# Performance work log

Hardware: AMD Instinct MI355X
Metric: run time of the kernel (lower is better)

Reference implementation:

```python
import jax, jax.numpy as jnp
import numpy as np
import math

N = 8192
F_DIM = 128
ALPHA_SLOPE = 0.2  # LeakyReLU negative slope from __init__ alpha


def setup_inputs() -> dict:
    key = jax.random.key(0)
    k1, k2, k3, k4, k5 = jax.random.split(key, 5)
    inp = jax.random.normal(k1, (N, F_DIM), dtype=jnp.float32)
    adj = (jax.random.uniform(k2, (N, N)) < 0.02).astype(jnp.float32)
    adj = adj.at[jnp.arange(N), jnp.arange(N)].set(1.0)
    h0 = jax.random.normal(k3, (N, F_DIM), dtype=jnp.float32)
    W = jax.random.normal(k4, (F_DIM, F_DIM), dtype=jnp.float32) * (1.414 * math.sqrt(6.0 / (2 * F_DIM)))
    a = jax.random.normal(k5, (2 * F_DIM, 1), dtype=jnp.float32) * (1.414 * math.sqrt(6.0 / (2 * F_DIM + 1)))
    return {"inp": inp, "adj": adj, "h0": h0, "W": W, "a": a,
            "lamda": 0.5, "alpha_mix": 0.1, "l": 1}


def reference(inp, adj, h0, W, a, lamda, alpha_mix, l):
    # h = inp @ W  -> (N, F)
    h = inp @ W
    # score(i,j) = leakyrelu([h_i, h_j] @ a) = leakyrelu(h_i@a1 + h_j@a2)
    # avoids materializing the O(N^2 * 2F) a_input tensor of the original
    f1 = h @ a[:F_DIM, 0]   # (N,)
    f2 = h @ a[F_DIM:, 0]   # (N,)
    e = jax.nn.leaky_relu(f1[:, None] + f2[None, :], negative_slope=ALPHA_SLOPE)  # (N, N)
    e = jnp.where(adj > 0, e, jnp.float32(-1e12))
    attention = jax.nn.softmax(e, axis=1)
    # dropout skipped (inference / training=False)
    hi = attention @ inp                      # (N, F) -- note: aggregates inp, not h
    support = (1.0 - alpha_mix) * hi + alpha_mix * h0
    theta = min(1.0, math.log(lamda / l + 1.0))
    output = theta * (support @ W) + (1.0 - theta) * support + inp
    return output
```

## Files before the change

### kernel.cpp

```cpp
#include <hip/hip_runtime.h>
#include <math.h>

#define N 8192
#define F 128
#define SLOPE 0.2f
#define SEGCAP 96
#define RPB 4

typedef float f4v __attribute__((ext_vector_type(4)));

__device__ __forceinline__ float lrelu(float x) { return x > 0.0f ? x : SLOPE * x; }

__device__ __forceinline__ f4v ntload(const float* p) {
    return __builtin_nontemporal_load(reinterpret_cast<const f4v*>(p));
}

__device__ __forceinline__ int mbcnt64(unsigned long long m) {
    return __builtin_amdgcn_mbcnt_hi((unsigned)(m >> 32),
                                     __builtin_amdgcn_mbcnt_lo((unsigned)m, 0u));
}

__device__ __forceinline__ unsigned bf16pair(float a, float b) {
    unsigned ua = __builtin_bit_cast(unsigned, a);
    unsigned ub = __builtin_bit_cast(unsigned, b);
    ua = (ua + 0x7FFFu + ((ua >> 16) & 1u)) >> 16;
    ub = (ub + 0x7FFFu + ((ub >> 16) & 1u)) >> 16;
    return ua | (ub << 16);
}
__device__ __forceinline__ float bflo(unsigned u) {
    return __builtin_bit_cast(float, u << 16);
}
__device__ __forceinline__ float bfhi(unsigned u) {
    return __builtin_bit_cast(float, u & 0xFFFF0000u);
}

__global__ __launch_bounds__(128) void k_wa(const float* __restrict__ W,
                                            const float* __restrict__ a,
                                            float* __restrict__ Wa1,
                                            float* __restrict__ Wa2) {
    const int k = threadIdx.x;
    const float* wr = W + k * F;
    float s1 = 0.f, s2 = 0.f;
    #pragma unroll 8
    for (int j = 0; j < F; ++j) {
        float w = wr[j];
        s1 += w * a[j];
        s2 += w * a[F + j];
    }
    Wa1[k] = s1;
    Wa2[k] = s2;
}

__global__ __launch_bounds__(256) void k_f(const float* __restrict__ inp,
                                           const float* __restrict__ Wa1,
                                           const float* __restrict__ Wa2,
                                           float* __restrict__ f1,
                                           float* __restrict__ f2,
                                           unsigned* __restrict__ inpb) {
    const int lane = threadIdx.x & 63;
    const int wv = threadIdx.x >> 6;
    const int i = blockIdx.x * 4 + wv;
    const float2 xv = *reinterpret_cast<const float2*>(inp + (size_t)i * F + 2 * lane);
    const float2 w1v = *reinterpret_cast<const float2*>(Wa1 + 2 * lane);
    const float2 w2v = *reinterpret_cast<const float2*>(Wa2 + 2 * lane);
    float v1 = xv.x * w1v.x + xv.y * w1v.y;
    float v2 = xv.x * w2v.x + xv.y * w2v.y;
    #pragma unroll
    for (int off = 32; off; off >>= 1) {
        v1 += __shfl_xor(v1, off);
        v2 += __shfl_xor(v2, off);
    }
    if (lane == 0) { f1[i] = v1; f2[i] = v2; }
    inpb[i * 64 + lane] = bf16pair(xv.x, xv.y);
}

__global__ __launch_bounds__(1024) void k_max(const float* __restrict__ f2,
                                              float* __restrict__ f2max) {
    float m = -INFINITY;
    for (int idx = threadIdx.x; idx < N; idx += 1024) m = fmaxf(m, f2[idx]);
    #pragma unroll
    for (int off = 32; off; off >>= 1) m = fmaxf(m, __shfl_xor(m, off));
    __shared__ float s[16];
    if ((threadIdx.x & 63) == 0) s[threadIdx.x >> 6] = m;
    __syncthreads();
    if (threadIdx.x == 0) {
        float r = s[0];
        #pragma unroll
        for (int t = 1; t < 16; ++t) r = fmaxf(r, s[t]);
        *f2max = r;
    }
}

__global__ __launch_bounds__(256, 8) void k_compact(const float* __restrict__ adj,
                                                    int* __restrict__ nzidx,
                                                    int* __restrict__ nzcnt) {
    const int row = blockIdx.x;
    const int wv = threadIdx.x >> 6;
    const int lane = threadIdx.x & 63;

    __shared__ int s_seg[4][SEGCAP];

    const float* base = adj + (size_t)row * N + wv * 2048 + lane * 4;
    f4v v[8];
    #pragma unroll
    for (int u = 0; u < 8; ++u) v[u] = ntload(base + u * 256);

    int cnt = 0;
    #pragma unroll
    for (int u = 0; u < 8; ++u) {
        const int col0 = wv * 2048 + u * 256 + lane * 4;
        #pragma unroll
        for (int c = 0; c < 4; ++c) {
            const bool nz = v[u][c] > 0.f;
            const unsigned long long m = __ballot(nz);
            const int pos = mbcnt64(m);
            int p = cnt + pos;
            if (p > SEGCAP - 1) p = SEGCAP - 1;
            if (nz) s_seg[wv][p] = col0 + c;
            cnt += (int)__popcll(m);
        }
    }
    const int M = cnt > SEGCAP ? SEGCAP : cnt;
    int* seg = nzidx + ((size_t)row * 4 + wv) * SEGCAP;
    for (int t2 = lane; t2 < M; t2 += 64) seg[t2] = s_seg[wv][t2];
    if (lane == 0) nzcnt[row * 4 + wv] = M;
}

__global__ __launch_bounds__(256, 8) void k_agg(const int* __restrict__ nzidx,
                                                const int* __restrict__ nzcnt,
                                                const unsigned* __restrict__ inpb,
                                                const float* __restrict__ inp,
                                                const float* __restrict__ h0,
                                                const float* __restrict__ W,
                                                const float* __restrict__ f1,
                                                const float* __restrict__ f2,
                                                const float* __restrict__ f2max_p,
                                                const float* __restrict__ lamda_p,
                                                const float* __restrict__ alpha_p,
                                                const int* __restrict__ l_p,
                                                float* __restrict__ out) {
    const int r0 = blockIdx.x * RPB;
    const int t = threadIdx.x;
    const int lane = t & 63;
    const int wv = t >> 6;
    const int i = r0 + wv;

    __shared__ int   s_j[RPB][392];
    __shared__ float s_w[RPB][392];
    __shared__ float s_sup[RPB][F];
    __shared__ float s_dot[RPB][F];

    const float f1i = f1[i];
    const float bound = lrelu(f1i + *f2max_p);

    int total = 0;
    float wlane = 0.f;
    #pragma unroll
    for (int s = 0; s < 4; ++s) {
        const int cnt = nzcnt[i * 4 + s];
        const int* seg = nzidx + ((size_t)i * 4 + s) * SEGCAP;
        const int e2 = 64 + lane;
        const int j1 = (lane < cnt) ? seg[lane] : -1;
        const int j2 = (e2 < cnt) ? seg[e2] : -1;
        float w1 = 0.f, w2 = 0.f;
        if (j1 >= 0) w1 = __expf(lrelu(f1i + f2[j1]) - bound);
        if (j2 >= 0) w2 = __expf(lrelu(f1i + f2[j2]) - bound);
        if (j1 >= 0) { s_j[wv][total + lane] = j1; s_w[wv][total + lane] = w1; }
        if (j2 >= 0) { s_j[wv][total + e2] = j2; s_w[wv][total + e2] = w2; }
        wlane += w1 + w2;
        total += cnt;
    }
    if (lane < 4) { s_j[wv][total + lane] = 0; s_w[wv][total + lane] = 0.f; }
    float wsum = wlane;
    #pragma unroll
    for (int off = 32; off; off >>= 1) wsum += __shfl_xor(wsum, off);

    float acc_e = 0.f, acc_o = 0.f;
    for (int e = 0; e < total; e += 4) {
        const int4  jv = *reinterpret_cast<const int4*>(&s_j[wv][e]);
        const f4v   wq = *reinterpret_cast<const f4v*>(&s_w[wv][e]);
        const unsigned a0 = inpb[(size_t)jv.x * 64 + lane];
        const unsigned a1 = inpb[(size_t)jv.y * 64 + lane];
        const unsigned a2 = inpb[(size_t)jv.z * 64 + lane];
        const unsigned a3 = inpb[(size_t)jv.w * 64 + lane];
        acc_e = fmaf(wq[0], bflo(a0), acc_e); acc_o = fmaf(wq[0], bfhi(a0), acc_o);
        acc_e = fmaf(wq[1], bflo(a1), acc_e); acc_o = fmaf(wq[1], bfhi(a1), acc_o);
        acc_e = fmaf(wq[2], bflo(a2), acc_e); acc_o = fmaf(wq[2], bfhi(a2), acc_o);
        acc_e = fmaf(wq[3], bflo(a3), acc_e); acc_o = fmaf(wq[3], bfhi(a3), acc_o);
    }

    const float inv = 1.0f / wsum;
    const float alpha = *alpha_p;
    const float2 hv = *reinterpret_cast<const float2*>(h0 + (size_t)i * F + 2 * lane);
    const float sup_e = (1.0f - alpha) * (acc_e * inv) + alpha * hv.x;
    const float sup_o = (1.0f - alpha) * (acc_o * inv) + alpha * hv.y;
    s_sup[wv][2 * lane]     = sup_e;
    s_sup[wv][2 * lane + 1] = sup_o;
    __syncthreads();

    const int c = t & 127;
    const int h = t >> 7;
    float d0 = 0.f, d1 = 0.f, d2 = 0.f, d3 = 0.f;
    const int k0 = 64 * h;
    #pragma unroll 4
    for (int k = k0; k < k0 + 64; ++k) {
        const float wk = W[k * F + c];
        d0 = fmaf(s_sup[0][k], wk, d0);
        d1 = fmaf(s_sup[1][k], wk, d1);
        d2 = fmaf(s_sup[2][k], wk, d2);
        d3 = fmaf(s_sup[3][k], wk, d3);
    }
    if (h == 0) {
        s_dot[0][c] = d0; s_dot[1][c] = d1; s_dot[2][c] = d2; s_dot[3][c] = d3;
    }
    __syncthreads();
    if (h == 1) {
        const float lam = *lamda_p;
        const float th = fminf(1.0f, logf(lam / (float)(*l_p) + 1.0f));
        const float dr[4] = { d0 + s_dot[0][c], d1 + s_dot[1][c],
                              d2 + s_dot[2][c], d3 + s_dot[3][c] };
        #pragma unroll
        for (int r = 0; r < RPB; ++r) {
            const size_t o = (size_t)(r0 + r) * F + c;
            out[o] = th * dr[r] + (1.0f - th) * s_sup[r][c] + inp[o];
        }
    }
}

extern "C" void kernel_launch(void* const* d_in, const int* in_sizes, int n_in,
                              void* d_out, int out_size, void* d_ws, size_t ws_size,
                              hipStream_t stream) {
    const float* inp   = (const float*)d_in[0];
    const float* adj   = (const float*)d_in[1];
    const float* h0    = (const float*)d_in[2];
    const float* W     = (const float*)d_in[3];
    const float* a     = (const float*)d_in[4];
    const float* lamda = (const float*)d_in[5];
    const float* alpha = (const float*)d_in[6];
    const int*   l     = (const int*)d_in[7];
    float* out = (float*)d_out;

    float* ws  = (float*)d_ws;
    float*    Wa1   = ws;
    float*    Wa2   = ws + F;
    float*    f1    = ws + 2 * F;
    float*    f2    = ws + 2 * F + N;
    float*    f2m   = ws + 2 * F + 2 * N;
    int*      nzcnt = (int*)(ws + 16704);
    int*      nzidx = (int*)(ws + 49472);
    unsigned* inpb  = (unsigned*)(ws + 3195200);

    hipLaunchKernelGGL(k_wa, dim3(1), dim3(F), 0, stream, W, a, Wa1, Wa2);
    hipLaunchKernelGGL(k_f, dim3(N / 4), dim3(256), 0, stream, inp, Wa1, Wa2, f1, f2, inpb);
    hipLaunchKernelGGL(k_max, dim3(1), dim3(1024), 0, stream, f2, f2m);
    hipLaunchKernelGGL(k_compact, dim3(N), dim3(256), 0, stream, adj, nzidx, nzcnt);
    hipLaunchKernelGGL(k_agg, dim3(N / RPB), dim3(256), 0, stream,
                       nzidx, nzcnt, inpb, inp, h0, W, f1, f2, f2m, lamda, alpha, l, out);
}
```

Baseline: 97.48 us.

## Merge compaction and feature-projection kernels, compute per-row softmax max in aggregation

The adjacency compaction and the f1/f2/bf16 projection kernels are fused into one launch, with block index selecting the role. The global f2 max reduction kernel is removed, and each row now computes its exact softmax max from its own neighbour scores before exponentiating. The k_wa kernel is parallelised over 256 threads using vector loads. The gather loop is unrolled to 8 neighbours per iteration, and the occupancy hint for k_agg is lowered. These changes cut launch count and serial single-block kernels at the cost of an extra max pass and more registers in the aggregation kernel.

```diff
diff --git a/kernel.cpp b/kernel.cpp
--- a/kernel.cpp
+++ b/kernel.cpp
@@ -34,99 +34,79 @@
     return __builtin_bit_cast(float, u & 0xFFFF0000u);
 }
 
-__global__ __launch_bounds__(128) void k_wa(const float* __restrict__ W,
+__global__ __launch_bounds__(256) void k_wa(const float* __restrict__ W,
                                             const float* __restrict__ a,
-                                            float* __restrict__ Wa1,
-                                            float* __restrict__ Wa2) {
-    const int k = threadIdx.x;
-    const float* wr = W + k * F;
-    float s1 = 0.f, s2 = 0.f;
-    #pragma unroll 8
-    for (int j = 0; j < F; ++j) {
-        float w = wr[j];
-        s1 += w * a[j];
-        s2 += w * a[F + j];
-    }
-    Wa1[k] = s1;
-    Wa2[k] = s2;
-}
-
-__global__ __launch_bounds__(256) void k_f(const float* __restrict__ inp,
-                                           const float* __restrict__ Wa1,
-                                           const float* __restrict__ Wa2,
-                                           float* __restrict__ f1,
-                                           float* __restrict__ f2,
-                                           unsigned* __restrict__ inpb) {
-    const int lane = threadIdx.x & 63;
-    const int wv = threadIdx.x >> 6;
-    const int i = blockIdx.x * 4 + wv;
-    const float2 xv = *reinterpret_cast<const float2*>(inp + (size_t)i * F + 2 * lane);
-    const float2 w1v = *reinterpret_cast<const float2*>(Wa1 + 2 * lane);
-    const float2 w2v = *reinterpret_cast<const float2*>(Wa2 + 2 * lane);
-    float v1 = xv.x * w1v.x + xv.y * w1v.y;
-    float v2 = xv.x * w2v.x + xv.y * w2v.y;
-    #pragma unroll
-    for (int off = 32; off; off >>= 1) {
-        v1 += __shfl_xor(v1, off);
-        v2 += __shfl_xor(v2, off);
-    }
-    if (lane == 0) { f1[i] = v1; f2[i] = v2; }
-    inpb[i * 64 + lane] = bf16pair(xv.x, xv.y);
-}
-
-__global__ __launch_bounds__(1024) void k_max(const float* __restrict__ f2,
-                                              float* __restrict__ f2max) {
-    float m = -INFINITY;
-    for (int idx = threadIdx.x; idx < N; idx += 1024) m = fmaxf(m, f2[idx]);
-    #pragma unroll
-    for (int off = 32; off; off >>= 1) m = fmaxf(m, __shfl_xor(m, off));
-    __shared__ float s[16];
-    if ((threadIdx.x & 63) == 0) s[threadIdx.x >> 6] = m;
-    __syncthreads();
-    if (threadIdx.x == 0) {
-        float r = s[0];
-        #pragma unroll
-        for (int t = 1; t < 16; ++t) r = fmaxf(r, s[t]);
-        *f2max = r;
-    }
-}
-
-__global__ __launch_bounds__(256, 8) void k_compact(const float* __restrict__ adj,
-                                                    int* __restrict__ nzidx,
-                                                    int* __restrict__ nzcnt) {
-    const int row = blockIdx.x;
+                                            float* __restrict__ Wa) {
+    const int t = threadIdx.x;
+    const int k = t & 127;
+    const int half = t >> 7;
+    const f4v* wr = reinterpret_cast<const f4v*>(W + k * F);
+    const f4v* av = reinterpret_cast<const f4v*>(a + half * F);
+    float s = 0.f;
+    #pragma unroll
+    for (int q = 0; q < 32; ++q) {
+        const f4v w = wr[q], aa = av[q];
+        s += (w[0] * aa[0] + w[1] * aa[1]) + (w[2] * aa[2] + w[3] * aa[3]);
+    }
+    Wa[t] = s;
+}
+
+__global__ __launch_bounds__(256, 8) void k_main(const float* __restrict__ adj,
+                                                 const float* __restrict__ inp,
+                                                 const float* __restrict__ Wa,
+                                                 float* __restrict__ f1,
+                                                 float* __restrict__ f2,
+                                                 unsigned* __restrict__ inpb,
+                                                 int* __restrict__ nzidx,
+                                                 int* __restrict__ nzcnt) {
+    __shared__ int s_seg[4][SEGCAP];
+    const int bid = blockIdx.x;
     const int wv = threadIdx.x >> 6;
     const int lane = threadIdx.x & 63;
 
-    __shared__ int s_seg[4][SEGCAP];
-
-    const float* base = adj + (size_t)row * N + wv * 2048 + lane * 4;
-    f4v v[8];
-    #pragma unroll
-    for (int u = 0; u < 8; ++u) v[u] = ntload(base + u * 256);
-
-    int cnt = 0;
-    #pragma unroll
-    for (int u = 0; u < 8; ++u) {
-        const int col0 = wv * 2048 + u * 256 + lane * 4;
-        #pragma unroll
-        for (int c = 0; c < 4; ++c) {
-            const bool nz = v[u][c] > 0.f;
-            const unsigned long long m = __ballot(nz);
-            const int pos = mbcnt64(m);
-            int p = cnt + pos;
-            if (p > SEGCAP - 1) p = SEGCAP - 1;
-            if (nz) s_seg[wv][p] = col0 + c;
-            cnt += (int)__popcll(m);
-        }
-    }
-    const int M = cnt > SEGCAP ? SEGCAP : cnt;
-    int* seg = nzidx + ((size_t)row * 4 + wv) * SEGCAP;
-    for (int t2 = lane; t2 < M; t2 += 64) seg[t2] = s_seg[wv][t2];
-    if (lane == 0) nzcnt[row * 4 + wv] = M;
-}
-
-__global__ __launch_bounds__(256, 8) void k_agg(const int* __restrict__ nzidx,
+    if (bid < N) {
+        const float* base = adj + (size_t)bid * N + wv * 2048 + lane * 4;
+        f4v v[8];
+        #pragma unroll
+        for (int u = 0; u < 8; ++u) v[u] = ntload(base + u * 256);
+
+        int cnt = 0;
+        #pragma unroll
+        for (int u = 0; u < 8; ++u) {
+            const int col0 = wv * 2048 + u * 256 + lane * 4;
+            #pragma unroll
+            for (int c = 0; c < 4; ++c) {
+                const bool nz = v[u][c] > 0.f;
+                const unsigned long long m = __ballot(nz);
+                const int pos = mbcnt64(m);
+                int p = cnt + pos;
+                if (p > SEGCAP - 1) p = SEGCAP - 1;
+                if (nz) s_seg[wv][p] = col0 + c;
+                cnt += (int)__popcll(m);
+            }
+        }
+        const int M = cnt > SEGCAP ? SEGCAP : cnt;
+        int* seg = nzidx + ((size_t)bid * 4 + wv) * SEGCAP;
+        for (int t2 = lane; t2 < M; t2 += 64) seg[t2] = s_seg[wv][t2];
+        if (lane == 0) nzcnt[bid * 4 + wv] = M;
+    } else {
+        const int i = (bid - N) * 4 + wv;
+        const float2 xv = *reinterpret_cast<const float2*>(inp + (size_t)i * F + 2 * lane);
+        const float2 w1v = *reinterpret_cast<const float2*>(Wa + 2 * lane);
+        const float2 w2v = *reinterpret_cast<const float2*>(Wa + F + 2 * lane);
+        float v1 = xv.x * w1v.x + xv.y * w1v.y;
+        float v2 = xv.x * w2v.x + xv.y * w2v.y;
+        #pragma unroll
+        for (int off = 32; off; off >>= 1) {
+            v1 += __shfl_xor(v1, off);
+            v2 += __shfl_xor(v2, off);
+        }
+        if (lane == 0) { f1[i] = v1; f2[i] = v2; }
+        inpb[i * 64 + lane] = bf16pair(xv.x, xv.y);
+    }
+}
+
+__global__ __launch_bounds__(256, 4) void k_agg(const int* __restrict__ nzidx,
                                                 const int* __restrict__ nzcnt,
                                                 const unsigned* __restrict__ inpb,
                                                 const float* __restrict__ inp,
@@ -134,7 +114,6 @@
                                                 const float* __restrict__ W,
                                                 const float* __restrict__ f1,
                                                 const float* __restrict__ f2,
-                                                const float* __restrict__ f2max_p,
                                                 const float* __restrict__ lamda_p,
                                                 const float* __restrict__ alpha_p,
                                                 const int* __restrict__ l_p,
@@ -145,48 +124,74 @@
     const int wv = t >> 6;
     const int i = r0 + wv;
 
-    __shared__ int   s_j[RPB][392];
-    __shared__ float s_w[RPB][392];
+    __shared__ int   s_j[RPB][400];
+    __shared__ float s_w[RPB][400];
     __shared__ float s_sup[RPB][F];
     __shared__ float s_dot[RPB][F];
 
     const float f1i = f1[i];
-    const float bound = lrelu(f1i + *f2max_p);
+
+    int cnts[4], jA[4], jB[4];
+    float sA[4], sB[4];
+    float mx = -1e30f;
+    #pragma unroll
+    for (int s = 0; s < 4; ++s) {
+        cnts[s] = nzcnt[i * 4 + s];
+        const int* seg = nzidx + ((size_t)i * 4 + s) * SEGCAP;
+        jA[s] = (lane < cnts[s]) ? seg[lane] : -1;
+        jB[s] = (64 + lane < cnts[s]) ? seg[64 + lane] : -1;
+        sA[s] = (jA[s] >= 0) ? lrelu(f1i + f2[jA[s]]) : -1e30f;
+        sB[s] = (jB[s] >= 0) ? lrelu(f1i + f2[jB[s]]) : -1e30f;
+        mx = fmaxf(mx, fmaxf(sA[s], sB[s]));
+    }
+    #pragma unroll
+    for (int off = 32; off; off >>= 1) mx = fmaxf(mx, __shfl_xor(mx, off));
 
     int total = 0;
     float wlane = 0.f;
     #pragma unroll
     for (int s = 0; s < 4; ++s) {
-        const int cnt = nzcnt[i * 4 + s];
-        const int* seg = nzidx + ((size_t)i * 4 + s) * SEGCAP;
-        const int e2 = 64 + lane;
-        const int j1 = (lane < cnt) ? seg[lane] : -1;
-        const int j2 = (e2 < cnt) ? seg[e2] : -1;
         float w1 = 0.f, w2 = 0.f;
-        if (j1 >= 0) w1 = __expf(lrelu(f1i + f2[j1]) - bound);
-        if (j2 >= 0) w2 = __expf(lrelu(f1i + f2[j2]) - bound);
-        if (j1 >= 0) { s_j[wv][total + lane] = j1; s_w[wv][total + lane] = w1; }
-        if (j2 >= 0) { s_j[wv][total + e2] = j2; s_w[wv][total + e2] = w2; }
+        if (jA[s] >= 0) {
+            w1 = __expf(sA[s] - mx);
+            s_j[wv][total + lane] = jA[s];
+            s_w[wv][total + lane] = w1;
+        }
+        if (jB[s] >= 0) {
+            w2 = __expf(sB[s] - mx);
+            s_j[wv][total + 64 + lane] = jB[s];
+            s_w[wv][total + 64 + lane] = w2;
+        }
         wlane += w1 + w2;
-        total += cnt;
-    }
-    if (lane < 4) { s_j[wv][total + lane] = 0; s_w[wv][total + lane] = 0.f; }
+        total += cnts[s];
+    }
+    if (lane < 8) { s_j[wv][total + lane] = 0; s_w[wv][total + lane] = 0.f; }
     float wsum = wlane;
     #pragma unroll
     for (int off = 32; off; off >>= 1) wsum += __shfl_xor(wsum, off);
 
     float acc_e = 0.f, acc_o = 0.f;
-    for (int e = 0; e < total; e += 4) {
-        const int4  jv = *reinterpret_cast<const int4*>(&s_j[wv][e]);
-        const f4v   wq = *reinterpret_cast<const f4v*>(&s_w[wv][e]);
-        const unsigned a0 = inpb[(size_t)jv.x * 64 + lane];
-        const unsigned a1 = inpb[(size_t)jv.y * 64 + lane];
-        const unsigned a2 = inpb[(size_t)jv.z * 64 + lane];
-        const unsigned a3 = inpb[(size_t)jv.w * 64 + lane];
-        acc_e = fmaf(wq[0], bflo(a0), acc_e); acc_o = fmaf(wq[0], bfhi(a0), acc_o);
-        acc_e = fmaf(wq[1], bflo(a1), acc_e); acc_o = fmaf(wq[1], bfhi(a1), acc_o);
-        acc_e = fmaf(wq[2], bflo(a2), acc_e); acc_o = fmaf(wq[2], bfhi(a2), acc_o);
-        acc_e = fmaf(wq[3], bflo(a3), acc_e); acc_o = fmaf(wq[3], bfhi(a3), acc_o);
+    for (int e = 0; e < total; e += 8) {
+        const int4 jv0 = *reinterpret_cast<const int4*>(&s_j[wv][e]);
+        const int4 jv1 = *reinterpret_cast<const int4*>(&s_j[wv][e + 4]);
+        const f4v  wq0 = *reinterpret_cast<const f4v*>(&s_w[wv][e]);
+        const f4v  wq1 = *reinterpret_cast<const f4v*>(&s_w[wv][e + 4]);
+        const unsigned a0 = inpb[(size_t)jv0.x * 64 + lane];
+        const unsigned a1 = inpb[(size_t)jv0.y * 64 + lane];
+        const unsigned a2 = inpb[(size_t)jv0.z * 64 + lane];
+        const unsigned a3 = inpb[(size_t)jv0.w * 64 + lane];
+        const unsigned a4 = inpb[(size_t)jv1.x * 64 + lane];
+        const unsigned a5 = inpb[(size_t)jv1.y * 64 + lane];
+        const unsigned a6 = inpb[(size_t)jv1.z * 64 + lane];
+        const unsigned a7 = inpb[(size_t)jv1.w * 64 + lane];
+        acc_e = fmaf(wq0[0], bflo(a0), acc_e); acc_o = fmaf(wq0[0], bfhi(a0), acc_o);
+        acc_e = fmaf(wq0[1], bflo(a1), acc_e); acc_o = fmaf(wq0[1], bfhi(a1), acc_o);
+        acc_e = fmaf(wq0[2], bflo(a2), acc_e); acc_o = fmaf(wq0[2], bfhi(a2), acc_o);
+        acc_e = fmaf(wq0[3], bflo(a3), acc_e); acc_o = fmaf(wq0[3], bfhi(a3), acc_o);
+        acc_e = fmaf(wq1[0], bflo(a4), acc_e); acc_o = fmaf(wq1[0], bfhi(a4), acc_o);
+        acc_e = fmaf(wq1[1], bflo(a5), acc_e); acc_o = fmaf(wq1[1], bfhi(a5), acc_o);
+        acc_e = fmaf(wq1[2], bflo(a6), acc_e); acc_o = fmaf(wq1[2], bfhi(a6), acc_o);
+        acc_e = fmaf(wq1[3], bflo(a7), acc_e); acc_o = fmaf(wq1[3], bfhi(a7), acc_o);
     }
 
     const float inv = 1.0f / wsum;
@@ -240,20 +245,17 @@
     const int*   l     = (const int*)d_in[7];
     float* out = (float*)d_out;
 
-    float* ws  = (float*)d_ws;
-    float*    Wa1   = ws;
-    float*    Wa2   = ws + F;
-    float*    f1    = ws + 2 * F;
-    float*    f2    = ws + 2 * F + N;
-    float*    f2m   = ws + 2 * F + 2 * N;
-    int*      nzcnt = (int*)(ws + 16704);
-    int*      nzidx = (int*)(ws + 49472);
-    unsigned* inpb  = (unsigned*)(ws + 3195200);
-
-    hipLaunchKernelGGL(k_wa, dim3(1), dim3(F), 0, stream, W, a, Wa1, Wa2);
-    hipLaunchKernelGGL(k_f, dim3(N / 4), dim3(256), 0, stream, inp, Wa1, Wa2, f1, f2, inpb);
-    hipLaunchKernelGGL(k_max, dim3(1), dim3(1024), 0, stream, f2, f2m);
-    hipLaunchKernelGGL(k_compact, dim3(N), dim3(256), 0, stream, adj, nzidx, nzcnt);
+    float* ws = (float*)d_ws;
+    float*    Wa    = ws;
+    float*    f1    = ws + 256;
+    float*    f2    = ws + 256 + N;
+    int*      nzcnt = (int*)(ws + 256 + 2 * N);
+    int*      nzidx = (int*)(ws + 49408);
+    unsigned* inpb  = (unsigned*)(ws + 3195136);
+
+    hipLaunchKernelGGL(k_wa, dim3(1), dim3(256), 0, stream, W, a, Wa);
+    hipLaunchKernelGGL(k_main, dim3(N + 2048), dim3(256), 0, stream,
+                       adj, inp, Wa, f1, f2, inpb, nzidx, nzcnt);
     hipLaunchKernelGGL(k_agg, dim3(N / RPB), dim3(256), 0, stream,
-                       nzidx, nzcnt, inpb, inp, h0, W, f1, f2, f2m, lamda, alpha, l, out);
-}
+                       nzidx, nzcnt, inpb, inp, h0, W, f1, f2, lamda, alpha, l, out);
+}
```

Measured after the change: 90.62 us. 1.08x faster.
